# Kernel optimization log

Hardware: AMD Instinct MI355X
Metric: run time of the kernel (lower is better)

Reference implementation:

```python
import jax, jax.numpy as jnp
import numpy as np

TEMPERATURE = 0.5
NEG_INF = -1e30


def setup_inputs() -> dict:
    key = jax.random.key(0)
    batch_size, k, d = 2048, 4, 256
    features = jax.random.normal(key, (batch_size * k, d), dtype=jnp.float32)
    return {"features": features, "batch_size": batch_size, "k": k}


def reference(features, batch_size, k):
    n = batch_size * k
    f = features.reshape(n, -1)
    f = f / jnp.linalg.norm(f, axis=1, keepdims=True)
    sim = jnp.matmul(f, f.T) / TEMPERATURE  # [N, N]

    gid = jnp.arange(n) // k
    eye = jnp.eye(n, dtype=bool)
    pos_mask = (gid[:, None] == gid[None, :]) & ~eye  # same image, not self
    all_mask = ~eye  # positives + negatives (everything except self)

    lse_pos = jax.nn.logsumexp(jnp.where(pos_mask, sim, NEG_INF), axis=1)
    lse_all = jax.nn.logsumexp(jnp.where(all_mask, sim, NEG_INF), axis=1)
    # every row has k-1 >= 1 positives, so all queries contribute
    return jnp.mean(-(lse_pos - lse_all))
```

## Files before the change

kernel.cpp:

```cpp
#include <hip/hip_runtime.h>
#include <math.h>

#define NROW 8192
#define DIM 256
#define NTILE 64
#define NBLK 2080
#define NT 24

typedef float f32x4  __attribute__((ext_vector_type(4)));
typedef short short8 __attribute__((ext_vector_type(8)));

__device__ __forceinline__ ushort f2bf_rne(float x) {
    unsigned u = __float_as_uint(x);
    unsigned r = (u + 0x7FFFu + ((u >> 16) & 1u)) >> 16;
    return (ushort)r;
}
__device__ __forceinline__ float bf2f(ushort h) {
    return __uint_as_float(((unsigned)h) << 16);
}

__global__ __launch_bounds__(256) void prep_kernel(const float* __restrict__ f,
                                                   ushort* __restrict__ Hi,
                                                   ushort* __restrict__ Lo,
                                                   float* __restrict__ sums) {
    if (threadIdx.x < 8) sums[blockIdx.x * 8 + threadIdx.x] = 0.0f;
    const int row = blockIdx.x * 4 + (threadIdx.x >> 6);
    const int l   = threadIdx.x & 63;
    float4 v = reinterpret_cast<const float4*>(f + (size_t)row * DIM)[l];
    float ss = v.x * v.x + v.y * v.y + v.z * v.z + v.w * v.w;
#pragma unroll
    for (int m = 32; m; m >>= 1) ss += __shfl_xor(ss, m, 64);
    const float inv = 1.0f / sqrtf(ss);
    float xv[4] = {v.x * inv, v.y * inv, v.z * inv, v.w * inv};
    ushort hv[4], lv[4];
#pragma unroll
    for (int i = 0; i < 4; ++i) {
        hv[i] = f2bf_rne(xv[i]);
        lv[i] = f2bf_rne(xv[i] - bf2f(hv[i]));
    }
    size_t idx = (size_t)((row >> 4) * 32 + (l >> 1)) * 128 + (row & 15) * 8 + (l & 1) * 4;
    *reinterpret_cast<ushort4*>(&Hi[idx]) = make_ushort4(hv[0], hv[1], hv[2], hv[3]);
    *reinterpret_cast<ushort4*>(&Lo[idx]) = make_ushort4(lv[0], lv[1], lv[2], lv[3]);
}

__device__ __forceinline__ void gload16(const void* g, void* lp) {
    __builtin_amdgcn_global_load_lds((__attribute__((address_space(1))) void*)g,
                                     (__attribute__((address_space(3))) void*)lp, 16, 0, 0);
}

__global__ __launch_bounds__(256, 3) void infonce_mfma(const ushort* __restrict__ Hi,
                                                       const ushort* __restrict__ Lo,
                                                       float* __restrict__ all_sum,
                                                       float* __restrict__ pos_sum) {
    __shared__ ushort lds[3][2][4096];

    int ti = 0, rem = blockIdx.x;
    while (rem >= NTILE - ti) { rem -= NTILE - ti; ++ti; }
    const int tj = ti + rem;

    const int tid = threadIdx.x;
    const int wid = tid >> 6, l = tid & 63;
    const int wr = wid >> 1, wc = wid & 1;

    f32x4 acc[4][4];
#pragma unroll
    for (int m = 0; m < 4; ++m)
#pragma unroll
        for (int n = 0; n < 4; ++n) acc[m][n] = (f32x4){0.f, 0.f, 0.f, 0.f};

#define STAGE(bufi, t) do {                                                             \
        const int pass_ = (t) >> 3, kk_ = (t) & 7;                                      \
        const ushort* As_ = (pass_ == 2) ? Lo : Hi;                                     \
        const ushort* Bs_ = (pass_ == 1) ? Lo : Hi;                                     \
        const int f0_ = wid * 2, f1_ = f0_ + 1;                                         \
        gload16(&As_[(size_t)((ti * 8 + f0_) * 4096 + kk_ * 512) + l * 8],              \
                &lds[bufi][0][f0_ * 512 + l * 8]);                                      \
        gload16(&As_[(size_t)((ti * 8 + f1_) * 4096 + kk_ * 512) + l * 8],              \
                &lds[bufi][0][f1_ * 512 + l * 8]);                                      \
        gload16(&Bs_[(size_t)((tj * 8 + f0_) * 4096 + kk_ * 512) + l * 8],              \
                &lds[bufi][1][f0_ * 512 + l * 8]);                                      \
        gload16(&Bs_[(size_t)((tj * 8 + f1_) * 4096 + kk_ * 512) + l * 8],              \
                &lds[bufi][1][f1_ * 512 + l * 8]);                                      \
    } while (0)

#define VWAIT(n) asm volatile("s_waitcnt vmcnt(" #n ")" ::: "memory")

#define BODY(t, bR, bS) do {                                                            \
        short8 af_[4], bf_[4];                                                          \
        _Pragma("unroll") for (int m = 0; m < 4; ++m)                                   \
            af_[m] = *reinterpret_cast<const short8*>(&lds[bR][0][(wr * 4 + m) * 512 + l * 8]); \
        _Pragma("unroll") for (int n = 0; n < 4; ++n)                                   \
            bf_[n] = *reinterpret_cast<const short8*>(&lds[bR][1][(wc * 4 + n) * 512 + l * 8]); \
        if ((t) + 2 < NT) STAGE(bS, (t) + 2);                                           \
        __builtin_amdgcn_s_setprio(1);                                                  \
        _Pragma("unroll") for (int m = 0; m < 4; ++m)                                   \
            _Pragma("unroll") for (int n = 0; n < 4; ++n)                               \
                acc[m][n] = __builtin_amdgcn_mfma_f32_16x16x32_bf16(af_[m], bf_[n], acc[m][n], 0, 0, 0); \
        __builtin_amdgcn_s_setprio(0);                                                  \
        if ((t) + 2 < NT) { VWAIT(4); } else { VWAIT(0); }                              \
        __builtin_amdgcn_s_barrier();                                                   \
    } while (0)

    STAGE(0, 0);
    STAGE(1, 1);
    VWAIT(4);
    __builtin_amdgcn_s_barrier();

#pragma unroll 1
    for (int tb = 0; tb < NT; tb += 3) {
        BODY(tb + 0, 0, 2);
        BODY(tb + 1, 1, 0);
        BODY(tb + 2, 2, 1);
    }

    const int rbase = ti * 128 + wr * 64;
    const int cbase = tj * 128 + wc * 64;
    const int h = l >> 4, c16 = l & 15;

    if (ti == tj) {
#pragma unroll
        for (int m = 0; m < 4; ++m)
#pragma unroll
            for (int e = 0; e < 4; ++e) {
                const int row = rbase + m * 16 + h * 4 + e;
                float asum = 0.f, psum = 0.f;
#pragma unroll
                for (int n = 0; n < 4; ++n) {
                    const int col = cbase + n * 16 + c16;
                    float v = __expf(2.0f * acc[m][n][e]);
                    v = (row == col) ? 0.f : v;
                    asum += v;
                    psum += ((row >> 2) == (col >> 2)) ? v : 0.f;
                }
#pragma unroll
                for (int mk = 1; mk < 16; mk <<= 1) {
                    asum += __shfl_xor(asum, mk, 64);
                    psum += __shfl_xor(psum, mk, 64);
                }
                if (c16 == 0) {
                    atomicAdd(&all_sum[row], asum);
                    atomicAdd(&pos_sum[row], psum);
                }
            }
    } else {
        float csum[4] = {0.f, 0.f, 0.f, 0.f};
#pragma unroll
        for (int m = 0; m < 4; ++m)
#pragma unroll
            for (int e = 0; e < 4; ++e) {
                const int row = rbase + m * 16 + h * 4 + e;
                float asum = 0.f;
#pragma unroll
                for (int n = 0; n < 4; ++n) {
                    float v = __expf(2.0f * acc[m][n][e]);
                    asum += v;
                    csum[n] += v;
                }
#pragma unroll
                for (int mk = 1; mk < 16; mk <<= 1) asum += __shfl_xor(asum, mk, 64);
                if (c16 == 0) atomicAdd(&all_sum[row], asum);
            }
#pragma unroll
        for (int n = 0; n < 4; ++n) {
            float cs = csum[n];
            cs += __shfl_xor(cs, 16, 64);
            cs += __shfl_xor(cs, 32, 64);
            if (h == 0) atomicAdd(&all_sum[cbase + n * 16 + c16], cs);
        }
    }
#undef STAGE
#undef VWAIT
#undef BODY
}

__global__ __launch_bounds__(1024) void loss_kernel(const float* __restrict__ all_sum,
                                                    const float* __restrict__ pos_sum,
                                                    float* __restrict__ out) {
    const int tid = threadIdx.x;
    float s = 0.0f;
#pragma unroll
    for (int r = 0; r < 8; ++r) {
        const int i = tid + r * 1024;
        s += __logf(all_sum[i]) - __logf(pos_sum[i]);
    }
#pragma unroll
    for (int off = 32; off; off >>= 1) s += __shfl_xor(s, off, 64);
    __shared__ float red[16];
    if ((tid & 63) == 0) red[tid >> 6] = s;
    __syncthreads();
    if (tid == 0) {
        float tot = 0.f;
#pragma unroll
        for (int i = 0; i < 16; ++i) tot += red[i];
        out[0] = tot / (float)NROW;
    }
}

extern "C" void kernel_launch(void* const* d_in, const int* in_sizes, int n_in,
                              void* d_out, int out_size, void* d_ws, size_t ws_size,
                              hipStream_t stream) {
    const float* f = (const float*)d_in[0];
    float* out = (float*)d_out;

    float*  all_sum = (float*)d_ws;
    float*  pos_sum = all_sum + NROW;
    ushort* Hi      = (ushort*)(pos_sum + NROW);
    ushort* Lo      = Hi + (size_t)NROW * DIM;

    prep_kernel<<<NROW / 4, 256, 0, stream>>>(f, Hi, Lo, all_sum);
    infonce_mfma<<<NBLK, 256, 0, stream>>>(Hi, Lo, all_sum, pos_sum);
    loss_kernel<<<1, 1024, 0, stream>>>(all_sum, pos_sum, out);
}
```

Before: 141.6 us.

## Use 256x256 tiles with 32x32x16 MFMA, 8 waves, and swizzled block order

Enlarges the symmetric output tile from 128x128 to 256x256, so only 528 upper-triangular blocks run. Each block now has 512 threads, and each wave computes a 128x64 sub-tile with 32x32x16 bf16 MFMA. The prep kernel writes Hi/Lo in plain row-major order and the LDS layout is built in-kernel, and block indices are swizzled so neighbouring blocks share tiles in cache. This roughly halves global and L2 operand traffic per FLOP and the number of atomics. In exchange, the grid of 528 blocks may underfill the 256 CUs at 2 blocks per CU, and register pressure rises with 128 accumulators per lane.

```diff
diff --git a/kernel.cpp b/kernel.cpp
--- a/kernel.cpp
+++ b/kernel.cpp
@@ -3,11 +3,11 @@
 
 #define NROW 8192
 #define DIM 256
-#define NTILE 64
-#define NBLK 2080
+#define NP 32
+#define NBLK 528
 #define NT 24
 
-typedef float f32x4  __attribute__((ext_vector_type(4)));
+typedef float f32x16 __attribute__((ext_vector_type(16)));
 typedef short short8 __attribute__((ext_vector_type(8)));
 
 __device__ __forceinline__ ushort f2bf_rne(float x) {
@@ -23,7 +23,7 @@
                                                    ushort* __restrict__ Hi,
                                                    ushort* __restrict__ Lo,
                                                    float* __restrict__ sums) {
-    if (threadIdx.x < 8) sums[blockIdx.x * 8 + threadIdx.x] = 0.0f;
+    if (blockIdx.x < 64) sums[blockIdx.x * 256 + threadIdx.x] = 0.0f;
     const int row = blockIdx.x * 4 + (threadIdx.x >> 6);
     const int l   = threadIdx.x & 63;
     float4 v = reinterpret_cast<const float4*>(f + (size_t)row * DIM)[l];
@@ -38,9 +38,8 @@
         hv[i] = f2bf_rne(xv[i]);
         lv[i] = f2bf_rne(xv[i] - bf2f(hv[i]));
     }
-    size_t idx = (size_t)((row >> 4) * 32 + (l >> 1)) * 128 + (row & 15) * 8 + (l & 1) * 4;
-    *reinterpret_cast<ushort4*>(&Hi[idx]) = make_ushort4(hv[0], hv[1], hv[2], hv[3]);
-    *reinterpret_cast<ushort4*>(&Lo[idx]) = make_ushort4(lv[0], lv[1], lv[2], lv[3]);
+    reinterpret_cast<ushort4*>(Hi + (size_t)row * DIM)[l] = make_ushort4(hv[0], hv[1], hv[2], hv[3]);
+    reinterpret_cast<ushort4*>(Lo + (size_t)row * DIM)[l] = make_ushort4(lv[0], lv[1], lv[2], lv[3]);
 }
 
 __device__ __forceinline__ void gload16(const void* g, void* lp) {
@@ -48,56 +47,66 @@
                                      (__attribute__((address_space(3))) void*)lp, 16, 0, 0);
 }
 
-__global__ __launch_bounds__(256, 3) void infonce_mfma(const ushort* __restrict__ Hi,
+__global__ __launch_bounds__(512, 2) void infonce_mfma(const ushort* __restrict__ Hi,
                                                        const ushort* __restrict__ Lo,
                                                        float* __restrict__ all_sum,
                                                        float* __restrict__ pos_sum) {
-    __shared__ ushort lds[3][2][4096];
-
-    int ti = 0, rem = blockIdx.x;
-    while (rem >= NTILE - ti) { rem -= NTILE - ti; ++ti; }
+    __shared__ ushort lds[3][16384];
+
+    const int swz = (blockIdx.x & 7) * 66 + (blockIdx.x >> 3);
+    int ti = 0, rem = swz;
+    while (rem >= NP - ti) { rem -= NP - ti; ++ti; }
     const int tj = ti + rem;
 
     const int tid = threadIdx.x;
     const int wid = tid >> 6, l = tid & 63;
-    const int wr = wid >> 1, wc = wid & 1;
-
-    f32x4 acc[4][4];
+    const int wr = wid >> 2, wc = wid & 3;
+    const int h = l >> 5, c32 = l & 31;
+    const int laneoff = (h << 8) + (c32 << 3);
+    const size_t aOff = (size_t)(ti * 256 + wid * 32 + c32) * DIM + h * 8;
+    const size_t bOff = (size_t)(tj * 256 + wid * 32 + c32) * DIM + h * 8;
+
+    f32x16 acc[4][2];
 #pragma unroll
     for (int m = 0; m < 4; ++m)
 #pragma unroll
-        for (int n = 0; n < 4; ++n) acc[m][n] = (f32x4){0.f, 0.f, 0.f, 0.f};
+        for (int n = 0; n < 2; ++n)
+#pragma unroll
+            for (int e = 0; e < 16; ++e) acc[m][n][e] = 0.0f;
 
 #define STAGE(bufi, t) do {                                                             \
-        const int pass_ = (t) >> 3, kk_ = (t) & 7;                                      \
+        const int pass_ = (t) >> 3, kb_ = ((t) & 7) * 32;                               \
         const ushort* As_ = (pass_ == 2) ? Lo : Hi;                                     \
         const ushort* Bs_ = (pass_ == 1) ? Lo : Hi;                                     \
-        const int f0_ = wid * 2, f1_ = f0_ + 1;                                         \
-        gload16(&As_[(size_t)((ti * 8 + f0_) * 4096 + kk_ * 512) + l * 8],              \
-                &lds[bufi][0][f0_ * 512 + l * 8]);                                      \
-        gload16(&As_[(size_t)((ti * 8 + f1_) * 4096 + kk_ * 512) + l * 8],              \
-                &lds[bufi][0][f1_ * 512 + l * 8]);                                      \
-        gload16(&Bs_[(size_t)((tj * 8 + f0_) * 4096 + kk_ * 512) + l * 8],              \
-                &lds[bufi][1][f0_ * 512 + l * 8]);                                      \
-        gload16(&Bs_[(size_t)((tj * 8 + f1_) * 4096 + kk_ * 512) + l * 8],              \
-                &lds[bufi][1][f1_ * 512 + l * 8]);                                      \
+        gload16(As_ + aOff + kb_,      &lds[bufi][(wid * 2 + 0) * 512 + laneoff]);      \
+        gload16(As_ + aOff + kb_ + 16, &lds[bufi][(wid * 2 + 1) * 512 + laneoff]);      \
+        gload16(Bs_ + bOff + kb_,      &lds[bufi][8192 + (wid * 2 + 0) * 512 + laneoff]); \
+        gload16(Bs_ + bOff + kb_ + 16, &lds[bufi][8192 + (wid * 2 + 1) * 512 + laneoff]); \
     } while (0)
 
 #define VWAIT(n) asm volatile("s_waitcnt vmcnt(" #n ")" ::: "memory")
 
-#define BODY(t, bR, bS) do {                                                            \
-        short8 af_[4], bf_[4];                                                          \
-        _Pragma("unroll") for (int m = 0; m < 4; ++m)                                   \
-            af_[m] = *reinterpret_cast<const short8*>(&lds[bR][0][(wr * 4 + m) * 512 + l * 8]); \
-        _Pragma("unroll") for (int n = 0; n < 4; ++n)                                   \
-            bf_[n] = *reinterpret_cast<const short8*>(&lds[bR][1][(wc * 4 + n) * 512 + l * 8]); \
-        if ((t) + 2 < NT) STAGE(bS, (t) + 2);                                           \
+#define BODY(t, bR, bS, DOSTG, W) do {                                                  \
+        const ushort* bp_ = lds[bR];                                                    \
+        short8 a0_[4], b0_[2], a1_[4], b1_[2];                                          \
+        _Pragma("unroll") for (int m = 0; m < 4; ++m)                                   \
+            a0_[m] = *(const short8*)&bp_[((wr * 4 + m) * 2 + 0) * 512 + laneoff];      \
+        _Pragma("unroll") for (int n = 0; n < 2; ++n)                                   \
+            b0_[n] = *(const short8*)&bp_[8192 + ((wc * 2 + n) * 2 + 0) * 512 + laneoff]; \
+        if (DOSTG) STAGE(bS, (t) + 2);                                                  \
+        _Pragma("unroll") for (int m = 0; m < 4; ++m)                                   \
+            a1_[m] = *(const short8*)&bp_[((wr * 4 + m) * 2 + 1) * 512 + laneoff];      \
+        _Pragma("unroll") for (int n = 0; n < 2; ++n)                                   \
+            b1_[n] = *(const short8*)&bp_[8192 + ((wc * 2 + n) * 2 + 1) * 512 + laneoff]; \
         __builtin_amdgcn_s_setprio(1);                                                  \
         _Pragma("unroll") for (int m = 0; m < 4; ++m)                                   \
-            _Pragma("unroll") for (int n = 0; n < 4; ++n)                               \
-                acc[m][n] = __builtin_amdgcn_mfma_f32_16x16x32_bf16(af_[m], bf_[n], acc[m][n], 0, 0, 0); \
+            _Pragma("unroll") for (int n = 0; n < 2; ++n)                               \
+                acc[m][n] = __builtin_amdgcn_mfma_f32_32x32x16_bf16(a0_[m], b0_[n], acc[m][n], 0, 0, 0); \
+        _Pragma("unroll") for (int m = 0; m < 4; ++m)                                   \
+            _Pragma("unroll") for (int n = 0; n < 2; ++n)                               \
+                acc[m][n] = __builtin_amdgcn_mfma_f32_32x32x16_bf16(a1_[m], b1_[n], acc[m][n], 0, 0, 0); \
         __builtin_amdgcn_s_setprio(0);                                                  \
-        if ((t) + 2 < NT) { VWAIT(4); } else { VWAIT(0); }                              \
+        VWAIT(W);                                                                       \
         __builtin_amdgcn_s_barrier();                                                   \
     } while (0)
 
@@ -107,65 +116,63 @@
     __builtin_amdgcn_s_barrier();
 
 #pragma unroll 1
-    for (int tb = 0; tb < NT; tb += 3) {
-        BODY(tb + 0, 0, 2);
-        BODY(tb + 1, 1, 0);
-        BODY(tb + 2, 2, 1);
-    }
-
-    const int rbase = ti * 128 + wr * 64;
-    const int cbase = tj * 128 + wc * 64;
-    const int h = l >> 4, c16 = l & 15;
+    for (int tb = 0; tb < 21; tb += 3) {
+        BODY(tb + 0, 0, 2, 1, 4);
+        BODY(tb + 1, 1, 0, 1, 4);
+        BODY(tb + 2, 2, 1, 1, 4);
+    }
+    BODY(21, 0, 2, 1, 4);
+    BODY(22, 1, 0, 0, 0);
+    BODY(23, 2, 0, 0, 0);
+
+    const int rb0 = ti * 256 + wr * 128;
+    const int cb0 = tj * 256 + wc * 64;
 
     if (ti == tj) {
 #pragma unroll
         for (int m = 0; m < 4; ++m)
 #pragma unroll
-            for (int e = 0; e < 4; ++e) {
-                const int row = rbase + m * 16 + h * 4 + e;
+            for (int e = 0; e < 16; ++e) {
+                const int row = rb0 + m * 32 + (e & 3) + 8 * (e >> 2) + 4 * h;
                 float asum = 0.f, psum = 0.f;
 #pragma unroll
-                for (int n = 0; n < 4; ++n) {
-                    const int col = cbase + n * 16 + c16;
+                for (int n = 0; n < 2; ++n) {
+                    const int col = cb0 + n * 32 + c32;
                     float v = __expf(2.0f * acc[m][n][e]);
                     v = (row == col) ? 0.f : v;
                     asum += v;
                     psum += ((row >> 2) == (col >> 2)) ? v : 0.f;
                 }
 #pragma unroll
-                for (int mk = 1; mk < 16; mk <<= 1) {
+                for (int mk = 1; mk < 32; mk <<= 1) {
                     asum += __shfl_xor(asum, mk, 64);
                     psum += __shfl_xor(psum, mk, 64);
                 }
-                if (c16 == 0) {
+                if (c32 == 0) {
                     atomicAdd(&all_sum[row], asum);
                     atomicAdd(&pos_sum[row], psum);
                 }
             }
     } else {
-        float csum[4] = {0.f, 0.f, 0.f, 0.f};
+        float cs0 = 0.f, cs1 = 0.f;
 #pragma unroll
         for (int m = 0; m < 4; ++m)
 #pragma unroll
-            for (int e = 0; e < 4; ++e) {
-                const int row = rbase + m * 16 + h * 4 + e;
-                float asum = 0.f;
-#pragma unroll
-                for (int n = 0; n < 4; ++n) {
-                    float v = __expf(2.0f * acc[m][n][e]);
-                    asum += v;
-                    csum[n] += v;
-                }
-#pragma unroll
-                for (int mk = 1; mk < 16; mk <<= 1) asum += __shfl_xor(asum, mk, 64);
-                if (c16 == 0) atomicAdd(&all_sum[row], asum);
+            for (int e = 0; e < 16; ++e) {
+                const int row = rb0 + m * 32 + (e & 3) + 8 * (e >> 2) + 4 * h;
+                float v0 = __expf(2.0f * acc[m][0][e]);
+                float v1 = __expf(2.0f * acc[m][1][e]);
+                cs0 += v0; cs1 += v1;
+                float asum = v0 + v1;
+#pragma unroll
+                for (int mk = 1; mk < 32; mk <<= 1) asum += __shfl_xor(asum, mk, 64);
+                if (c32 == 0) atomicAdd(&all_sum[row], asum);
             }
-#pragma unroll
-        for (int n = 0; n < 4; ++n) {
-            float cs = csum[n];
-            cs += __shfl_xor(cs, 16, 64);
-            cs += __shfl_xor(cs, 32, 64);
-            if (h == 0) atomicAdd(&all_sum[cbase + n * 16 + c16], cs);
+        cs0 += __shfl_xor(cs0, 32, 64);
+        cs1 += __shfl_xor(cs1, 32, 64);
+        if (h == 0) {
+            atomicAdd(&all_sum[cb0 + c32], cs0);
+            atomicAdd(&all_sum[cb0 + 32 + c32], cs1);
         }
     }
 #undef STAGE
@@ -208,6 +215,6 @@
     ushort* Lo      = Hi + (size_t)NROW * DIM;
 
     prep_kernel<<<NROW / 4, 256, 0, stream>>>(f, Hi, Lo, all_sum);
-    infonce_mfma<<<NBLK, 256, 0, stream>>>(Hi, Lo, all_sum, pos_sum);
+    infonce_mfma<<<NBLK, 512, 0, stream>>>(Hi, Lo, all_sum, pos_sum);
     loss_kernel<<<1, 1024, 0, stream>>>(all_sum, pos_sum, out);
 }
```

Result: slower. 270.9 us (+91.2%).
